# Performance work log

Measured on AMD Instinct MI355X. Metric: run time of the kernel, lower is better.

## Reference

```python
import jax, jax.numpy as jnp
import numpy as np

N, H, DDE, NH = 256, 256, 64, 4

def setup_inputs() -> dict:
    key = jax.random.key(0)
    ks = jax.random.split(key, 12)
    rn = lambda k, s, sc=1.0: (jax.random.normal(k, s) * sc).astype(jnp.float32)
    return {
        "action_hidden_state": rn(ks[0], (N, H)),
        "goal_hidden_state": rn(ks[1], (N, H)),
        "goal": rn(ks[2], (N, 2)),
        "action": rn(ks[3], (N, 2)),
        "W_dist": rn(ks[4], (8, DDE), 0.3),          # distEmbedding Linear(8, dde)
        "b_dist": jnp.zeros((DDE,), jnp.float32),
        "W_gate": rn(ks[5], (DDE, H), 0.1),          # gateFC Linear(dde, H)
        "b_gate": jnp.zeros((H,), jnp.float32),
        "w": rn(ks[6], (NH, 1, H, H), 0.06),         # GAT per-head projection
        "a": rn(ks[7], (1, 1, 2 * H, 1), 0.06),      # attention vector
        "bias": jnp.zeros((H,), jnp.float32),
    }

def reference(action_hidden_state, goal_hidden_state, goal, action,
              W_dist, b_dist, W_gate, b_gate, w, a, bias):
    n = goal.shape[0]
    # --- InteractionGate.cal_gate: x1[i,j] = x[j], x2[i,j] = x[i] ---
    g1 = jnp.broadcast_to(goal[None, :, :], (n, n, 2))
    g2 = jnp.broadcast_to(goal[:, None, :], (n, n, 2))
    a1 = jnp.broadcast_to(action[None, :, :], (n, n, 2))
    a2 = jnp.broadcast_to(action[:, None, :], (n, n, 2))
    dist = jnp.concatenate([a2, g2, a1, g1], axis=-1)                 # [n,n,8]
    gate = jax.nn.sigmoid(jax.nn.relu(dist @ W_dist + b_dist) @ W_gate + b_gate)  # [n,n,H]
    # temp_action_1[i,j] = action_hidden_state[j]
    gate_action = gate * jnp.tanh(action_hidden_state[None, :, :])    # [n,n,H]
    # diagonal entries replaced by goal_hidden_state (mask_goal = eye)
    eye = jnp.eye(n, dtype=bool)[:, :, None]
    gated_h = jnp.where(eye, goal_hidden_state[None, :, :], gate_action)  # [n,n,H]

    # --- GAT assembly: h_self[i,k] = ahs[i]; h_other = cat(ahs, gated_h) ---
    h_other = jnp.concatenate([action_hidden_state[:, None, :], gated_h], axis=1)  # [n,n+1,H]

    wm = w[:, 0]          # [NH,H,H]
    a_flat = a[0, 0, :, 0]  # [2H]
    f = wm.shape[-1]
    n_head = wm.shape[0]
    # h_self rows along k are all identical -> project once per (head, node)
    hsp = jnp.einsum('nh,zhf->znf', action_hidden_state, wm)          # [NH,n,f]
    hop = jnp.einsum('nkh,zhf->znkf', h_other, wm)                    # [NH,n,n+1,f]
    # cat([h_self', h_other']) @ a  ==  h_self'@a[:f] + h_other'@a[f:]
    score = (hsp @ a_flat[:f])[:, :, None] + hop @ a_flat[f:]         # [NH,n,n+1]
    e = jnp.where(score > 0, score, 0.2 * score)                      # LeakyReLU(0.2)
    alpha = jax.nn.softmax(e, axis=-1)                                # softmax over neighbors
    # h_attn = matmul(h_other, w) == hop; weighted sum over k, mean over heads
    out = jnp.einsum('znk,znkf->nf', alpha, hop) / n_head             # [n,f]
    return jax.nn.relu(out) + bias
```

## Files before the change

### kernel.cpp

```cpp
#include <hip/hip_runtime.h>
#include <hip/hip_bf16.h>

#define NN 256
#define HH 256

typedef __attribute__((ext_vector_type(8))) short short8;
typedef __attribute__((ext_vector_type(4))) float f32x4;

__device__ __forceinline__ ushort f2bf(float x) {
    __hip_bfloat16 h = __float2bfloat16(x);
    return *reinterpret_cast<ushort*>(&h);
}
__device__ __forceinline__ float bf2f(ushort u) {
    __hip_bfloat16 h = *reinterpret_cast<__hip_bfloat16*>(&u);
    return __bfloat162float(h);
}
template <int CTRL>
__device__ __forceinline__ float dpp_add(float x) {
    int y = __builtin_amdgcn_update_dpp(0, __float_as_int(x), CTRL, 0xF, 0xF, true);
    return x + __int_as_float(y);
}
template <int CTRL>
__device__ __forceinline__ float dpp_max(float x) {
    int y = __builtin_amdgcn_update_dpp(0, __float_as_int(x), CTRL, 0xF, 0xF, true);
    return fmaxf(x, __int_as_float(y));
}
__device__ __forceinline__ float red16(float v) {
    v = dpp_add<0xB1>(v); v = dpp_add<0x4E>(v);
    v = dpp_add<0x141>(v); v = dpp_add<0x140>(v);
    return v;
}
__device__ __forceinline__ float red16max(float v) {
    v = dpp_max<0xB1>(v); v = dpp_max<0x4E>(v);
    v = dpp_max<0x141>(v); v = dpp_max<0x140>(v);
    return v;
}

#define WS_P   0
#define WS_Q   16384
#define WS_T   32768
#define WS_WA  98304
#define WS_WB  99328
#define WS_WGT 100352
#define WS_PV  108544
#define WS_ML  632832
#define WS_W2H 636928
#define WS_W2L 768000

__global__ __launch_bounds__(256) void precompute_kernel(
    const float* __restrict__ ahs, const float* __restrict__ goal,
    const float* __restrict__ action, const float* __restrict__ Wd,
    const float* __restrict__ b_dist, const float* __restrict__ Wg,
    const float* __restrict__ w, const float* __restrict__ a,
    float* __restrict__ ws)
{
    const int b = blockIdx.x;
    const int t = threadIdx.x;
    const int wid  = t >> 6;
    const int lane = t & 63;
    float* P  = ws + WS_P;
    float* Q  = ws + WS_Q;
    float* T  = ws + WS_T;
    float* WA = ws + WS_WA;
    float* WB = ws + WS_WB;
    ushort* WgT  = (ushort*)(ws + WS_WGT);
    ushort* W2hi = (ushort*)(ws + WS_W2H);
    ushort* W2lo = (ushort*)(ws + WS_W2L);

    __shared__ __align__(16) float tile[64][65];

    if (b < 16) {
        const int z  = b >> 2;
        const int rg = b & 3;
        const int hbase = rg*64 + wid*16;
        const f32x4 aB = *(const f32x4*)(a + lane*4);
        const f32x4 aA = *(const f32x4*)(a + HH + lane*4);
#pragma unroll 4
        for (int rr = 0; rr < 16; ++rr) {
            const int h = hbase + rr;
            const f32x4 w4 = *(const f32x4*)(w + z*HH*HH + h*HH + lane*4);
            float dA = w4.x*aA.x + w4.y*aA.y + w4.z*aA.z + w4.w*aA.w;
            float dB = w4.x*aB.x + w4.y*aB.y + w4.z*aB.z + w4.w*aB.w;
#pragma unroll
            for (int off = 32; off; off >>= 1) {
                dA += __shfl_xor(dA, off);
                dB += __shfl_xor(dB, off);
            }
            if (lane == 0) { WA[z*HH + h] = dA; WB[z*HH + h] = dB; }
        }
    } else if (b < 80) {
        const int idx = b - 16;
        const int k0  = (idx >> 2) * 64;
        const int f0  = (idx & 3) * 64;
        const int ff  = t & 63;
#pragma unroll 4
        for (int i = 0; i < 16; ++i) {
            const int kk = i*4 + wid;
            tile[kk][ff] = w[(k0 + kk)*HH + f0 + ff];
        }
        __syncthreads();
#pragma unroll 4
        for (int i = 0; i < 16; ++i) {
            const int fl = i*4 + wid;
            float x = tile[ff][fl];
            ushort hi = f2bf(x);
            ushort lo = f2bf(x - bf2f(hi));
            W2hi[(size_t)(f0 + fl)*1024 + k0 + ff] = hi;
            W2lo[(size_t)(f0 + fl)*1024 + k0 + ff] = lo;
        }
    } else if (b < 144) {
        const int i = (b - 80)*4 + wid;
        const int d = lane;
        float a0 = action[2*i], a1 = action[2*i+1];
        float g0 = goal[2*i],   g1 = goal[2*i+1];
        P[i*64 + d] = a0*Wd[0*64+d] + a1*Wd[1*64+d]
                    + g0*Wd[2*64+d] + g1*Wd[3*64+d] + b_dist[d];
        Q[i*64 + d] = a0*Wd[4*64+d] + a1*Wd[5*64+d]
                    + g0*Wd[6*64+d] + g1*Wd[7*64+d];
    } else if (b < 208) {
        const int d = b - 144;
        WgT[t*64 + d] = f2bf(Wg[d*HH + t]);
    } else {
        const int idx = ((b - 208)*256 + t)*4;
        float4 v = *(const float4*)(ahs + idx);
        float4 o;
        o.x = tanhf(v.x); o.y = tanhf(v.y); o.z = tanhf(v.z); o.w = tanhf(v.w);
        *(float4*)(T + idx) = o;
    }
}

__global__ __launch_bounds__(256, 2) void gat_partial_kernel(
    const float* __restrict__ ahs, const float* __restrict__ ghs,
    const float* __restrict__ b_gate, float* __restrict__ ws)
{
    const int n    = blockIdx.x >> 1;
    const int hh   = blockIdx.x & 1;
    const int t    = threadIdx.x;
    const int wid  = t >> 6;
    const int lane = t & 63;
    const int quad = lane >> 4;
    const int l15  = lane & 15;
    const int zg   = quad;
    const int jj   = l15;
    const int n0   = wid * 64;

    const float* P  = ws + WS_P;
    const float* Q  = ws + WS_Q;
    const float* T  = ws + WS_T;
    const float* WA = ws + WS_WA;
    const float* WB = ws + WS_WB;
    const ushort* WgT = (const ushort*)(ws + WS_WGT);
    float* PV = ws + WS_PV;
    float* ML = ws + WS_ML;

    __shared__ __align__(16) float part[2][4][16][4];
    __shared__ __align__(16) float alpha_w[4][16][4];
    __shared__ __align__(16) float vred[16][260];

    int hcol[4];
#pragma unroll
    for (int nt = 0; nt < 4; ++nt) hcol[nt] = n0 + nt*16 + l15;

    short8 bfrag[4][2];
    float  wa_reg[4][4];
    float  bgv[4], gval[4];
#pragma unroll
    for (int nt = 0; nt < 4; ++nt) {
#pragma unroll
        for (int kh = 0; kh < 2; ++kh)
            bfrag[nt][kh] = *(const short8*)(WgT + hcol[nt]*64 + kh*32 + quad*8);
#pragma unroll
        for (int z = 0; z < 4; ++z) wa_reg[z][nt] = WA[z*HH + hcol[nt]];
        bgv[nt]  = b_gate[hcol[nt]];
        gval[nt] = ghs[n*HH + hcol[nt]];
    }

    float pnA[2][8];
#pragma unroll
    for (int kh = 0; kh < 2; ++kh) {
        *(f32x4*)&pnA[kh][0] = *(const f32x4*)(P + n*64 + kh*32 + quad*8);
        *(f32x4*)&pnA[kh][4] = *(const f32x4*)(P + n*64 + kh*32 + quad*8 + 4);
    }

    float vacc[4][4];
    {
        float av[4];
#pragma unroll
        for (int nt = 0; nt < 4; ++nt) av[nt] = ahs[n*HH + hcol[nt]];
#pragma unroll
        for (int z = 0; z < 4; ++z)
#pragma unroll
            for (int nt = 0; nt < 4; ++nt)
                vacc[z][nt] = (hh == 0 && quad == 0) ? av[nt] : 0.f;
    }

    float cz_r, m_r, l_r;
    {
        float pc = 0.f, ps = 0.f;
        const int hb = jj*16;
#pragma unroll
        for (int i4 = 0; i4 < 4; ++i4) {
            f32x4 av = *(const f32x4*)(ahs + n*HH + hb + i4*4);
            f32x4 wb = *(const f32x4*)(WB + zg*HH + hb + i4*4);
            f32x4 wa = *(const f32x4*)(WA + zg*HH + hb + i4*4);
            pc = fmaf(av.x, wb.x, pc); pc = fmaf(av.y, wb.y, pc);
            pc = fmaf(av.z, wb.z, pc); pc = fmaf(av.w, wb.w, pc);
            ps = fmaf(av.x, wa.x, ps); ps = fmaf(av.y, wa.y, ps);
            ps = fmaf(av.z, wa.z, ps); ps = fmaf(av.w, wa.w, ps);
        }
        pc = red16(pc); ps = red16(ps);
        cz_r = pc;
        if (hh == 0) {
            float sc = pc + ps;
            m_r = sc > 0.f ? sc : 0.2f * sc;
            l_r = 1.0f;
        } else {
            m_r = -__builtin_inff();
            l_r = 0.0f;
        }
    }

    for (int cc = 0; cc < 8; ++cc) {
        const int j0  = hh*128 + cc*16;
        const int par = cc & 1;

        float tval[4][4];
#pragma unroll
        for (int r = 0; r < 4; ++r) {
            const int jg = j0 + quad*4 + r;
#pragma unroll
            for (int nt = 0; nt < 4; ++nt)
                tval[nt][r] = T[jg*HH + hcol[nt]];
        }

        short8 afrag[2];
#pragma unroll
        for (int kh = 0; kh < 2; ++kh) {
            const float* qrow = Q + (j0 + l15)*64 + kh*32 + quad*8;
            f32x4 qa = *(const f32x4*)qrow;
            f32x4 qb = *(const f32x4*)(qrow + 4);
            ushort hv[8];
            hv[0] = f2bf(fmaxf(pnA[kh][0] + qa.x, 0.f));
            hv[1] = f2bf(fmaxf(pnA[kh][1] + qa.y, 0.f));
            hv[2] = f2bf(fmaxf(pnA[kh][2] + qa.z, 0.f));
            hv[3] = f2bf(fmaxf(pnA[kh][3] + qa.w, 0.f));
            hv[4] = f2bf(fmaxf(pnA[kh][4] + qb.x, 0.f));
            hv[5] = f2bf(fmaxf(pnA[kh][5] + qb.y, 0.f));
            hv[6] = f2bf(fmaxf(pnA[kh][6] + qb.z, 0.f));
            hv[7] = f2bf(fmaxf(pnA[kh][7] + qb.w, 0.f));
            afrag[kh] = *(short8*)hv;
        }

        f32x4 acc[4];
#pragma unroll
        for (int nt = 0; nt < 4; ++nt) {
            f32x4 a4 = (f32x4){0.f,0.f,0.f,0.f};
            a4 = __builtin_amdgcn_mfma_f32_16x16x32_bf16(afrag[0], bfrag[nt][0], a4, 0, 0, 0);
            a4 = __builtin_amdgcn_mfma_f32_16x16x32_bf16(afrag[1], bfrag[nt][1], a4, 0, 0, 0);
            acc[nt] = a4;
        }

        float vals[4][4];
#pragma unroll
        for (int r = 0; r < 4; ++r) {
            const int jg = j0 + quad*4 + r;
            const bool diag = (jg == n);
#pragma unroll
            for (int nt = 0; nt < 4; ++nt) {
                float u = acc[nt][r] + bgv[nt];
                float g = 1.0f / (1.0f + __expf(-u));
                vals[nt][r] = diag ? gval[nt] : g * tval[nt][r];
            }
        }

#pragma unroll
        for (int z = 0; z < 4; ++z) {
            float pp[4];
#pragma unroll
            for (int r = 0; r < 4; ++r) {
                float s = 0.f;
#pragma unroll
                for (int nt = 0; nt < 4; ++nt)
                    s = fmaf(vals[nt][r], wa_reg[z][nt], s);
                pp[r] = red16(s);
            }
            if (l15 == z) {
#pragma unroll
                for (int r = 0; r < 4; ++r)
                    part[par][z][quad*4 + r][wid] = pp[r];
            }
        }
        __syncthreads();

        float scl0, scl1, scl2, scl3;
        {
            f32x4 pr = *(const f32x4*)&part[par][zg][jj][0];
            float s = cz_r + ((pr.x + pr.y) + (pr.z + pr.w));
            float e = s > 0.f ? s : 0.2f * s;
            float mx = red16max(e);
            float m_new = fmaxf(m_r, mx);
            float at = __expf(e - m_new);
            float ss = red16(at);
            float scale = __expf(m_r - m_new);
            l_r = l_r * scale + ss;
            m_r = m_new;
            alpha_w[wid][jj][zg] = at;
            scl0 = __shfl(scale, 0);
            scl1 = __shfl(scale, 16);
            scl2 = __shfl(scale, 32);
            scl3 = __shfl(scale, 48);
        }
#pragma unroll
        for (int nt = 0; nt < 4; ++nt) {
            vacc[0][nt] *= scl0; vacc[1][nt] *= scl1;
            vacc[2][nt] *= scl2; vacc[3][nt] *= scl3;
        }
#pragma unroll
        for (int r = 0; r < 4; ++r) {
            f32x4 al = *(const f32x4*)&alpha_w[wid][quad*4 + r][0];
#pragma unroll
            for (int nt = 0; nt < 4; ++nt) {
                float v = vals[nt][r];
                vacc[0][nt] = fmaf(al.x, v, vacc[0][nt]);
                vacc[1][nt] = fmaf(al.y, v, vacc[1][nt]);
                vacc[2][nt] = fmaf(al.z, v, vacc[2][nt]);
                vacc[3][nt] = fmaf(al.w, v, vacc[3][nt]);
            }
        }
    }

#pragma unroll
    for (int z = 0; z < 4; ++z)
#pragma unroll
        for (int nt = 0; nt < 4; ++nt)
            vred[quad*4 + z][hcol[nt]] = vacc[z][nt];
    __syncthreads();
#pragma unroll
    for (int z = 0; z < 4; ++z) {
        float s = (vred[0*4+z][t] + vred[1*4+z][t]) + (vred[2*4+z][t] + vred[3*4+z][t]);
        PV[((size_t)(hh*4 + z)*NN + n)*HH + t] = s;
    }
    if (wid == 0 && l15 == 0) {
        ML[((hh*4 + zg)*NN + n)*2 + 0] = m_r;
        ML[((hh*4 + zg)*NN + n)*2 + 1] = l_r;
    }
}

__global__ __launch_bounds__(256) void gat_out_kernel(
    const float* __restrict__ bias, const float* __restrict__ ws,
    float* __restrict__ out)
{
    const int n0 = (blockIdx.x >> 2) * 16;
    const int f0 = (blockIdx.x & 3) * 64;
    const int t    = threadIdx.x;
    const int wid  = t >> 6;
    const int lane = t & 63;
    const int quad = lane >> 4;
    const int l15  = lane & 15;

    const float* PV = ws + WS_PV;
    const float* ML = ws + WS_ML;
    const ushort* W2hi = (const ushort*)(ws + WS_W2H);
    const ushort* W2lo = (const ushort*)(ws + WS_W2L);

    __shared__ __align__(16) float redc[12288/4];
    __shared__ __align__(16) float sq[16][4][2];

    if (t < 128) {
        const int n_i = t >> 3, z = (t >> 1) & 3, q = t & 1;
        float m = ML[((q*4 + z)*NN + n0 + n_i)*2 + 0];
        float l = ML[((q*4 + z)*NN + n0 + n_i)*2 + 1];
        float mm = fmaxf(m, __shfl_xor(m, 1));
        float s  = __expf(m - mm);
        float ls = l * s;
        ls += __shfl_xor(ls, 1);
        sq[n_i][z][q] = s / ls;
    }
    __syncthreads();

    f32x4 acc[4];
#pragma unroll
    for (int nt = 0; nt < 4; ++nt) acc[nt] = (f32x4){0.f,0.f,0.f,0.f};

    const float s0 = sq[l15][wid][0];
    const float s1 = sq[l15][wid][1];
    const float* pv0 = PV + ((size_t)(0*4 + wid)*NN + n0 + l15)*HH;
    const float* pv1 = PV + ((size_t)(1*4 + wid)*NN + n0 + l15)*HH;

    for (int ks = 0; ks < 8; ++ks) {
        const int kp = ks*32 + quad*8;
        f32x4 p0a = *(const f32x4*)(pv0 + kp);
        f32x4 p0b = *(const f32x4*)(pv0 + kp + 4);
        f32x4 p1a = *(const f32x4*)(pv1 + kp);
        f32x4 p1b = *(const f32x4*)(pv1 + kp + 4);
        float v[8];
        v[0] = s0*p0a.x + s1*p1a.x; v[1] = s0*p0a.y + s1*p1a.y;
        v[2] = s0*p0a.z + s1*p1a.z; v[3] = s0*p0a.w + s1*p1a.w;
        v[4] = s0*p0b.x + s1*p1b.x; v[5] = s0*p0b.y + s1*p1b.y;
        v[6] = s0*p0b.z + s1*p1b.z; v[7] = s0*p0b.w + s1*p1b.w;
        ushort hi[8], lo[8];
#pragma unroll
        for (int c = 0; c < 8; ++c) {
            hi[c] = f2bf(v[c]);
            lo[c] = f2bf(v[c] - bf2f(hi[c]));
        }
        short8 ah = *(short8*)hi;
        short8 al = *(short8*)lo;
        const int kg = wid*256 + kp;
#pragma unroll
        for (int nt = 0; nt < 4; ++nt) {
            const size_t boff = (size_t)(f0 + nt*16 + l15)*1024 + kg;
            short8 bh = *(const short8*)(W2hi + boff);
            short8 bl = *(const short8*)(W2lo + boff);
            acc[nt] = __builtin_amdgcn_mfma_f32_16x16x32_bf16(ah, bh, acc[nt], 0, 0, 0);
            acc[nt] = __builtin_amdgcn_mfma_f32_16x16x32_bf16(ah, bl, acc[nt], 0, 0, 0);
            acc[nt] = __builtin_amdgcn_mfma_f32_16x16x32_bf16(al, bh, acc[nt], 0, 0, 0);
        }
    }
    __syncthreads();

    if (wid > 0) {
#pragma unroll
        for (int nt = 0; nt < 4; ++nt)
#pragma unroll
            for (int r = 0; r < 4; ++r)
                redc[(((wid-1)*4 + nt)*16 + quad*4 + r)*16 + l15] = acc[nt][r];
    }
    __syncthreads();
    if (wid == 0) {
#pragma unroll
        for (int nt = 0; nt < 4; ++nt) {
            const int f = f0 + nt*16 + l15;
            float bv = bias[f];
#pragma unroll
            for (int r = 0; r < 4; ++r) {
                const int row = quad*4 + r;
                float s = acc[nt][r]
                        + redc[((0*4 + nt)*16 + row)*16 + l15]
                        + redc[((1*4 + nt)*16 + row)*16 + l15]
                        + redc[((2*4 + nt)*16 + row)*16 + l15];
                out[(size_t)(n0 + row)*HH + f] = fmaxf(0.25f * s, 0.f) + bv;
            }
        }
    }
}

extern "C" void kernel_launch(void* const* d_in, const int* in_sizes, int n_in,
                              void* d_out, int out_size, void* d_ws, size_t ws_size,
                              hipStream_t stream)
{
    const float* ahs    = (const float*)d_in[0];
    const float* ghs    = (const float*)d_in[1];
    const float* goal   = (const float*)d_in[2];
    const float* action = (const float*)d_in[3];
    const float* Wd     = (const float*)d_in[4];
    const float* b_dist = (const float*)d_in[5];
    const float* Wg     = (const float*)d_in[6];
    const float* b_gate = (const float*)d_in[7];
    const float* w      = (const float*)d_in[8];
    const float* a      = (const float*)d_in[9];
    const float* bias   = (const float*)d_in[10];
    float* ws   = (float*)d_ws;
    float* outp = (float*)d_out;

    precompute_kernel<<<272, 256, 0, stream>>>(ahs, goal, action, Wd, b_dist, Wg, w, a, ws);
    gat_partial_kernel<<<512, 256, 0, stream>>>(ahs, ghs, b_gate, ws);
    gat_out_kernel<<<64, 256, 0, stream>>>(bias, ws, outp);
}
```

Measured before the change: 125.6 us.

## Stage gate A-fragments in LDS, prefetch T, fast math, widen output grid

Precomputes the whole block's relu(P+Q) bf16 A-matrix once into swizzled shared memory instead of rebuilding fragments every chunk iteration, and software-prefetches the next chunk's tanh values while the softmax step runs. Replaces tanhf and divisions with exp/rcp-based fast approximations. Splits the output GEMM kernel into 256 blocks of 16 features each, so more CUs are busy. This adds 16KB of LDS per block, which may reduce occupancy, and uses less precise tanh/reciprocal.

Result: faster. 114.6 us (median of 3 runs) (-8.8%).

```diff
diff --git a/kernel.cpp b/kernel.cpp
--- a/kernel.cpp
+++ b/kernel.cpp
@@ -14,6 +14,13 @@
 __device__ __forceinline__ float bf2f(ushort u) {
     __hip_bfloat16 h = *reinterpret_cast<__hip_bfloat16*>(&u);
     return __bfloat162float(h);
+}
+__device__ __forceinline__ float fast_rcp(float x) {
+    return __builtin_amdgcn_rcpf(x);
+}
+__device__ __forceinline__ float fast_tanh(float x) {
+    float e = __expf(2.0f * x);
+    return 1.0f - 2.0f * fast_rcp(e + 1.0f);
 }
 template <int CTRL>
 __device__ __forceinline__ float dpp_add(float x) {
@@ -124,7 +131,8 @@
         const int idx = ((b - 208)*256 + t)*4;
         float4 v = *(const float4*)(ahs + idx);
         float4 o;
-        o.x = tanhf(v.x); o.y = tanhf(v.y); o.z = tanhf(v.z); o.w = tanhf(v.w);
+        o.x = fast_tanh(v.x); o.y = fast_tanh(v.y);
+        o.z = fast_tanh(v.z); o.w = fast_tanh(v.w);
         *(float4*)(T + idx) = o;
     }
 }
@@ -156,6 +164,7 @@
     __shared__ __align__(16) float part[2][4][16][4];
     __shared__ __align__(16) float alpha_w[4][16][4];
     __shared__ __align__(16) float vred[16][260];
+    __shared__ __align__(16) ushort A_l[128*64];
 
     int hcol[4];
 #pragma unroll
@@ -175,11 +184,28 @@
         gval[nt] = ghs[n*HH + hcol[nt]];
     }
 
-    float pnA[2][8];
-#pragma unroll
-    for (int kh = 0; kh < 2; ++kh) {
-        *(f32x4*)&pnA[kh][0] = *(const f32x4*)(P + n*64 + kh*32 + quad*8);
-        *(f32x4*)&pnA[kh][4] = *(const f32x4*)(P + n*64 + kh*32 + quad*8 + 4);
+    {
+        const int jl = t >> 1;
+        const int kh = t & 1;
+        const float* prow = P + n*64 + kh*32;
+        const float* qrow = Q + (hh*128 + jl)*64 + kh*32;
+        ushort hv[32];
+#pragma unroll
+        for (int c = 0; c < 8; ++c) {
+            f32x4 pq = *(const f32x4*)(prow + c*4);
+            f32x4 qq = *(const f32x4*)(qrow + c*4);
+            hv[c*4+0] = f2bf(fmaxf(pq.x + qq.x, 0.f));
+            hv[c*4+1] = f2bf(fmaxf(pq.y + qq.y, 0.f));
+            hv[c*4+2] = f2bf(fmaxf(pq.z + qq.z, 0.f));
+            hv[c*4+3] = f2bf(fmaxf(pq.w + qq.w, 0.f));
+        }
+        char* rb = (char*)A_l + jl*128;
+        const int sw = (jl & 7) << 4;
+#pragma unroll
+        for (int c2 = 0; c2 < 4; ++c2) {
+            const int off = (kh*64 + c2*16) ^ sw;
+            *(short8*)(rb + off) = *(const short8*)(hv + c2*8);
+        }
     }
 
     float vacc[4][4];
@@ -220,43 +246,36 @@
         }
     }
 
+    __syncthreads();
+
+    float tval[4][4];
+    {
+        const int j0 = hh*128;
+#pragma unroll
+        for (int r = 0; r < 4; ++r) {
+            const int jg = j0 + quad*4 + r;
+#pragma unroll
+            for (int nt = 0; nt < 4; ++nt)
+                tval[nt][r] = T[jg*HH + hcol[nt]];
+        }
+    }
+
     for (int cc = 0; cc < 8; ++cc) {
         const int j0  = hh*128 + cc*16;
         const int par = cc & 1;
 
-        float tval[4][4];
-#pragma unroll
-        for (int r = 0; r < 4; ++r) {
-            const int jg = j0 + quad*4 + r;
-#pragma unroll
-            for (int nt = 0; nt < 4; ++nt)
-                tval[nt][r] = T[jg*HH + hcol[nt]];
-        }
-
-        short8 afrag[2];
-#pragma unroll
-        for (int kh = 0; kh < 2; ++kh) {
-            const float* qrow = Q + (j0 + l15)*64 + kh*32 + quad*8;
-            f32x4 qa = *(const f32x4*)qrow;
-            f32x4 qb = *(const f32x4*)(qrow + 4);
-            ushort hv[8];
-            hv[0] = f2bf(fmaxf(pnA[kh][0] + qa.x, 0.f));
-            hv[1] = f2bf(fmaxf(pnA[kh][1] + qa.y, 0.f));
-            hv[2] = f2bf(fmaxf(pnA[kh][2] + qa.z, 0.f));
-            hv[3] = f2bf(fmaxf(pnA[kh][3] + qa.w, 0.f));
-            hv[4] = f2bf(fmaxf(pnA[kh][4] + qb.x, 0.f));
-            hv[5] = f2bf(fmaxf(pnA[kh][5] + qb.y, 0.f));
-            hv[6] = f2bf(fmaxf(pnA[kh][6] + qb.z, 0.f));
-            hv[7] = f2bf(fmaxf(pnA[kh][7] + qb.w, 0.f));
-            afrag[kh] = *(short8*)hv;
-        }
+        const int jl = cc*16 + l15;
+        const char* rb = (const char*)A_l + jl*128;
+        const int sw = (l15 & 7) << 4;
+        short8 afrag0 = *(const short8*)(rb + ((quad*16) ^ sw));
+        short8 afrag1 = *(const short8*)(rb + ((64 + quad*16) ^ sw));
 
         f32x4 acc[4];
 #pragma unroll
         for (int nt = 0; nt < 4; ++nt) {
             f32x4 a4 = (f32x4){0.f,0.f,0.f,0.f};
-            a4 = __builtin_amdgcn_mfma_f32_16x16x32_bf16(afrag[0], bfrag[nt][0], a4, 0, 0, 0);
-            a4 = __builtin_amdgcn_mfma_f32_16x16x32_bf16(afrag[1], bfrag[nt][1], a4, 0, 0, 0);
+            a4 = __builtin_amdgcn_mfma_f32_16x16x32_bf16(afrag0, bfrag[nt][0], a4, 0, 0, 0);
+            a4 = __builtin_amdgcn_mfma_f32_16x16x32_bf16(afrag1, bfrag[nt][1], a4, 0, 0, 0);
             acc[nt] = a4;
         }
 
@@ -268,7 +287,7 @@
 #pragma unroll
             for (int nt = 0; nt < 4; ++nt) {
                 float u = acc[nt][r] + bgv[nt];
-                float g = 1.0f / (1.0f + __expf(-u));
+                float g = fast_rcp(1.0f + __expf(-u));
                 vals[nt][r] = diag ? gval[nt] : g * tval[nt][r];
             }
         }
@@ -291,6 +310,18 @@
             }
         }
         __syncthreads();
+
+        float tnext[4][4];
+        if (cc < 7) {
+            const int j1 = j0 + 16;
+#pragma unroll
+            for (int r = 0; r < 4; ++r) {
+                const int jg = j1 + quad*4 + r;
+#pragma unroll
+                for (int nt = 0; nt < 4; ++nt)
+                    tnext[nt][r] = T[jg*HH + hcol[nt]];
+            }
+        }
 
         float scl0, scl1, scl2, scl3;
         {
@@ -327,6 +358,13 @@
                 vacc[3][nt] = fmaf(al.w, v, vacc[3][nt]);
             }
         }
+        if (cc < 7) {
+#pragma unroll
+            for (int nt = 0; nt < 4; ++nt)
+#pragma unroll
+                for (int r = 0; r < 4; ++r)
+                    tval[nt][r] = tnext[nt][r];
+        }
     }
 
 #pragma unroll
@@ -350,8 +388,8 @@
     const float* __restrict__ bias, const float* __restrict__ ws,
     float* __restrict__ out)
 {
-    const int n0 = (blockIdx.x >> 2) * 16;
-    const int f0 = (blockIdx.x & 3) * 64;
+    const int n0 = (blockIdx.x >> 4) * 16;
+    const int f0 = (blockIdx.x & 15) * 16;
     const int t    = threadIdx.x;
     const int wid  = t >> 6;
     const int lane = t & 63;
@@ -363,7 +401,7 @@
     const ushort* W2hi = (const ushort*)(ws + WS_W2H);
     const ushort* W2lo = (const ushort*)(ws + WS_W2L);
 
-    __shared__ __align__(16) float redc[12288/4];
+    __shared__ __align__(16) float redc[3][16][17];
     __shared__ __align__(16) float sq[16][4][2];
 
     if (t < 128) {
@@ -374,13 +412,11 @@
         float s  = __expf(m - mm);
         float ls = l * s;
         ls += __shfl_xor(ls, 1);
-        sq[n_i][z][q] = s / ls;
+        sq[n_i][z][q] = s * fast_rcp(ls);
     }
     __syncthreads();
 
-    f32x4 acc[4];
-#pragma unroll
-    for (int nt = 0; nt < 4; ++nt) acc[nt] = (f32x4){0.f,0.f,0.f,0.f};
+    f32x4 acc = (f32x4){0.f,0.f,0.f,0.f};
 
     const float s0 = sq[l15][wid][0];
     const float s1 = sq[l15][wid][1];
@@ -406,41 +442,31 @@
         }
         short8 ah = *(short8*)hi;
         short8 al = *(short8*)lo;
-        const int kg = wid*256 + kp;
-#pragma unroll
-        for (int nt = 0; nt < 4; ++nt) {
-            const size_t boff = (size_t)(f0 + nt*16 + l15)*1024 + kg;
-            short8 bh = *(const short8*)(W2hi + boff);
-            short8 bl = *(const short8*)(W2lo + boff);
-            acc[nt] = __builtin_amdgcn_mfma_f32_16x16x32_bf16(ah, bh, acc[nt], 0, 0, 0);
-            acc[nt] = __builtin_amdgcn_mfma_f32_16x16x32_bf16(ah, bl, acc[nt], 0, 0, 0);
-            acc[nt] = __builtin_amdgcn_mfma_f32_16x16x32_bf16(al, bh, acc[nt], 0, 0, 0);
-        }
-    }
-    __syncthreads();
+        const size_t boff = (size_t)(f0 + l15)*1024 + wid*256 + kp;
+        short8 bh = *(const short8*)(W2hi + boff);
+        short8 bl = *(const short8*)(W2lo + boff);
+        acc = __builtin_amdgcn_mfma_f32_16x16x32_bf16(ah, bh, acc, 0, 0, 0);
+        acc = __builtin_amdgcn_mfma_f32_16x16x32_bf16(ah, bl, acc, 0, 0, 0);
+        acc = __builtin_amdgcn_mfma_f32_16x16x32_bf16(al, bh, acc, 0, 0, 0);
+    }
 
     if (wid > 0) {
 #pragma unroll
-        for (int nt = 0; nt < 4; ++nt)
-#pragma unroll
-            for (int r = 0; r < 4; ++r)
-                redc[(((wid-1)*4 + nt)*16 + quad*4 + r)*16 + l15] = acc[nt][r];
+        for (int r = 0; r < 4; ++r)
+            redc[wid-1][quad*4 + r][l15] = acc[r];
     }
     __syncthreads();
     if (wid == 0) {
-#pragma unroll
-        for (int nt = 0; nt < 4; ++nt) {
-            const int f = f0 + nt*16 + l15;
-            float bv = bias[f];
-#pragma unroll
-            for (int r = 0; r < 4; ++r) {
-                const int row = quad*4 + r;
-                float s = acc[nt][r]
-                        + redc[((0*4 + nt)*16 + row)*16 + l15]
-                        + redc[((1*4 + nt)*16 + row)*16 + l15]
-                        + redc[((2*4 + nt)*16 + row)*16 + l15];
-                out[(size_t)(n0 + row)*HH + f] = fmaxf(0.25f * s, 0.f) + bv;
-            }
+        const int f = f0 + l15;
+        float bv = bias[f];
+#pragma unroll
+        for (int r = 0; r < 4; ++r) {
+            const int row = quad*4 + r;
+            float s = acc[r]
+                    + redc[0][row][l15]
+                    + redc[1][row][l15]
+                    + redc[2][row][l15];
+            out[(size_t)(n0 + row)*HH + f] = fmaxf(0.25f * s, 0.f) + bv;
         }
     }
 }
@@ -465,5 +491,5 @@
 
     precompute_kernel<<<272, 256, 0, stream>>>(ahs, goal, action, Wd, b_dist, Wg, w, a, ws);
     gat_partial_kernel<<<512, 256, 0, stream>>>(ahs, ghs, b_gate, ws);
-    gat_out_kernel<<<64, 256, 0, stream>>>(bias, ws, outp);
-}
+    gat_out_kernel<<<256, 256, 0, stream>>>(bias, ws, outp);
+}
```
